# Kernel optimization log

Hardware: AMD Instinct MI355X
Metric: run time of the kernel (lower is better)

## Reference

```python
import jax, jax.numpy as jnp
import numpy as np
import math

B, N, D = 4, 16384, 256
M, H = 64, 8
HD = D // H

def setup_inputs() -> dict:
    key = jax.random.key(0)
    ks = jax.random.split(key, 5)
    s = 1.0 / math.sqrt(D)
    return {
        "x": jax.random.normal(ks[0], (B, N, D), dtype=jnp.float32),
        "Ws": jax.random.normal(ks[1], (M, D), dtype=jnp.float32) * s,
        "bs": jnp.zeros((M,), dtype=jnp.float32),
        "Wqkv": jax.random.normal(ks[2], (3 * D, D), dtype=jnp.float32) * s,
        "Wo": jax.random.normal(ks[3], (D, D), dtype=jnp.float32) * s,
        "bo": jnp.zeros((D,), dtype=jnp.float32),
    }

def reference(x, Ws, bs, Wqkv, Wo, bo):
    # slice weights: softmax over N (dim=1), matching the torch code exactly
    logits = jnp.einsum('bnd,md->bnm', x, Ws) + bs          # [B,N,M]
    weights = jax.nn.softmax(logits, axis=1)                # softmax over N
    # pooling: tokens[b,m,d] = sum_n w[b,n,m] * x[b,n,d]
    tokens = jnp.einsum('bnm,bnd->bmd', weights, x)         # [B,M,D]
    # qkv projection (no bias)
    qkv = jnp.einsum('bmd,ed->bme', tokens, Wqkv)           # [B,M,3D]
    qkv = qkv.reshape(B, M, 3, H, HD)
    q = qkv[:, :, 0].transpose(0, 2, 1, 3)                  # [B,H,M,HD]
    k = qkv[:, :, 1].transpose(0, 2, 1, 3)
    v = qkv[:, :, 2].transpose(0, 2, 1, 3)
    scale = 1.0 / math.sqrt(HD)
    attn = jax.nn.softmax(jnp.einsum('bhmd,bhkd->bhmk', q, k) * scale, axis=-1)
    token_out = jnp.einsum('bhmk,bhkd->bhmd', attn, v)      # [B,H,M,HD]
    token_out = token_out.transpose(0, 2, 1, 3).reshape(B, M, D)
    token_out = jnp.einsum('bmd,ed->bme', token_out, Wo) + bo
    # unpooling: out[b,n,d] = sum_m w[b,n,m] * token_out[b,m,d]
    out = jnp.einsum('bnm,bmd->bnd', weights, token_out)    # [B,N,D]
    return out
```

## Files before the change

### kernel.cpp

```cpp
#include <hip/hip_runtime.h>
#include <math.h>

constexpr int B = 4;
constexpr int N = 16384;
constexpr int D = 256;
constexpr int M = 64;
constexpr int H = 8;

typedef __attribute__((ext_vector_type(8))) short short8;
typedef __attribute__((ext_vector_type(4))) float floatx4;

__device__ __forceinline__ float4 ld4(const float* p) {
  return *reinterpret_cast<const float4*>(p);
}
__device__ __forceinline__ unsigned short f2bf(float f) {
  unsigned u = __float_as_uint(f);
  unsigned r = (u + 0x7fffu + ((u >> 16) & 1u)) >> 16;
  return (unsigned short)r;
}

__global__ __launch_bounds__(256) void k0_prep(
    const float* __restrict__ Ws, const float* __restrict__ Wqkv,
    const float* __restrict__ Wo, unsigned short* __restrict__ WsB,
    unsigned short* __restrict__ WqkvB, unsigned short* __restrict__ WoB) {
  const int g = blockIdx.x * 256 + threadIdx.x;
  const float* src;
  unsigned short* dst;
  int off;
  if (g < 2048) {
    src = Ws; dst = WsB; off = g;
  } else if (g < 26624) {
    src = Wqkv; dst = WqkvB; off = g - 2048;
  } else {
    src = Wo; dst = WoB; off = g - 26624;
  }
  const float4 a = ld4(&src[(size_t)off * 8]);
  const float4 c = ld4(&src[(size_t)off * 8 + 4]);
  unsigned d0 = (unsigned)f2bf(a.x) | ((unsigned)f2bf(a.y) << 16);
  unsigned d1 = (unsigned)f2bf(a.z) | ((unsigned)f2bf(a.w) << 16);
  unsigned d2 = (unsigned)f2bf(c.x) | ((unsigned)f2bf(c.y) << 16);
  unsigned d3 = (unsigned)f2bf(c.z) | ((unsigned)f2bf(c.w) << 16);
  *reinterpret_cast<uint4*>(&dst[(size_t)off * 8]) = make_uint4(d0, d1, d2, d3);
}

__global__ __launch_bounds__(256, 3) void k1_fused(
    const float* __restrict__ x, const unsigned short* __restrict__ WsB,
    const float* __restrict__ bs, unsigned short* __restrict__ En,
    float* __restrict__ denom) {
  __shared__ unsigned short Wt[64][264];
  __shared__ unsigned short Es[64][72];
  __shared__ float red[64];
  const int b = blockIdx.y;
  const int n0 = blockIdx.x * 64;
  const int tid = threadIdx.x;
  const int w = tid >> 6, l = tid & 63;
  const int l15 = l & 15;
  const int q8 = (l >> 4) * 8;
  const int ar = w * 16 + l15;

  float4 fx[16];
  const float* xrow = &x[((size_t)(b * N + n0 + ar)) * D];
#pragma unroll
  for (int ks = 0; ks < 8; ++ks) {
    fx[2 * ks] = ld4(&xrow[ks * 32 + q8]);
    fx[2 * ks + 1] = ld4(&xrow[ks * 32 + q8 + 4]);
  }
#pragma unroll
  for (int p = 0; p < 8; ++p) {
    const int u = p * 256 + tid;
    const int row = u >> 5;
    const int c = (u & 31) * 8;
    *reinterpret_cast<short8*>(&Wt[row][c]) =
        *reinterpret_cast<const short8*>(&WsB[(size_t)row * 256 + c]);
  }
  if (tid < 64) red[tid] = 0.0f;
  __syncthreads();

  short8 afr[8];
#pragma unroll
  for (int ks = 0; ks < 8; ++ks) {
    const float4 a0 = fx[2 * ks], a1 = fx[2 * ks + 1];
    short8 t;
    t[0] = (short)f2bf(a0.x); t[1] = (short)f2bf(a0.y);
    t[2] = (short)f2bf(a0.z); t[3] = (short)f2bf(a0.w);
    t[4] = (short)f2bf(a1.x); t[5] = (short)f2bf(a1.y);
    t[6] = (short)f2bf(a1.z); t[7] = (short)f2bf(a1.w);
    afr[ks] = t;
  }

  floatx4 acc[4] = {{0.f, 0.f, 0.f, 0.f},
                    {0.f, 0.f, 0.f, 0.f},
                    {0.f, 0.f, 0.f, 0.f},
                    {0.f, 0.f, 0.f, 0.f}};
#pragma unroll
  for (int ks = 0; ks < 8; ++ks) {
#pragma unroll
    for (int mt = 0; mt < 4; ++mt) {
      short8 bf = *reinterpret_cast<short8*>(&Wt[mt * 16 + l15][ks * 32 + q8]);
      acc[mt] = __builtin_amdgcn_mfma_f32_16x16x32_bf16(afr[ks], bf, acc[mt], 0, 0, 0);
    }
  }

#pragma unroll
  for (int mt = 0; mt < 4; ++mt) {
    const int m = mt * 16 + l15;
    const float bsm = bs[m];
    float s = 0.0f;
#pragma unroll
    for (int r = 0; r < 4; ++r) {
      const int n = w * 16 + (l >> 4) * 4 + r;
      const float e = expf(acc[mt][r] + bsm);
      s += e;
      Es[n][m] = f2bf(e);
    }
    atomicAdd(&red[m], s);
  }
  __syncthreads();
  if (tid < 64) atomicAdd(&denom[b * M + tid], red[tid]);
#pragma unroll
  for (int p = 0; p < 2; ++p) {
    const int g = p * 256 + tid;
    const int n = g >> 3;
    const int m0 = (g & 7) * 8;
    short8 v = *reinterpret_cast<short8*>(&Es[n][m0]);
    *reinterpret_cast<short8*>(&En[((size_t)(b * N + n0 + n)) * M + m0]) = v;
  }
}

__global__ __launch_bounds__(256) void k2_pool(
    const unsigned short* __restrict__ En, const float* __restrict__ x,
    float* __restrict__ tokens) {
  __shared__ unsigned short Ens[64][66];
  __shared__ unsigned short Xs[64][66];
  const int dt = blockIdx.x, nc = blockIdx.y, b = blockIdx.z;
  const int d0 = dt * 64;
  const int tid = threadIdx.x;
  const int w = tid >> 6, l = tid & 63;
  const int l15 = l & 15;
  const int q8 = (l >> 4) * 8;
  floatx4 acc[4] = {{0.f, 0.f, 0.f, 0.f},
                    {0.f, 0.f, 0.f, 0.f},
                    {0.f, 0.f, 0.f, 0.f},
                    {0.f, 0.f, 0.f, 0.f}};
  for (int kc = 0; kc < 8; ++kc) {
    const int nb = nc * 512 + kc * 64;
    __syncthreads();
#pragma unroll
    for (int p = 0; p < 2; ++p) {
      const int u = p * 256 + tid;
      const int n = u >> 3;
      const int c8 = (u & 7) * 8;
      short8 v = *reinterpret_cast<const short8*>(
          &En[((size_t)(b * N + nb + n)) * M + c8]);
      uint4 uv = *reinterpret_cast<uint4*>(&v);
      unsigned* dp = reinterpret_cast<unsigned*>(&Ens[n][c8]);
      dp[0] = uv.x; dp[1] = uv.y; dp[2] = uv.z; dp[3] = uv.w;
    }
    {
      const int n = tid >> 2;
      const int c16 = (tid & 3) * 16;
      const float* xp = &x[((size_t)(b * N + nb + n)) * D + d0 + c16];
#pragma unroll
      for (int q = 0; q < 4; ++q) {
        float4 v = ld4(xp + q * 4);
        unsigned u0 = (unsigned)f2bf(v.x) | ((unsigned)f2bf(v.y) << 16);
        unsigned u1 = (unsigned)f2bf(v.z) | ((unsigned)f2bf(v.w) << 16);
        unsigned* dp = reinterpret_cast<unsigned*>(&Xs[n][c16 + q * 4]);
        dp[0] = u0; dp[1] = u1;
      }
    }
    __syncthreads();
#pragma unroll
    for (int ks = 0; ks < 2; ++ks) {
      const int nf = ks * 32 + q8;
      short8 a;
#pragma unroll
      for (int j = 0; j < 8; ++j) a[j] = (short)Ens[nf + j][w * 16 + l15];
#pragma unroll
      for (int dtile = 0; dtile < 4; ++dtile) {
        short8 bf;
#pragma unroll
        for (int j = 0; j < 8; ++j) bf[j] = (short)Xs[nf + j][dtile * 16 + l15];
        acc[dtile] =
            __builtin_amdgcn_mfma_f32_16x16x32_bf16(a, bf, acc[dtile], 0, 0, 0);
      }
    }
  }
#pragma unroll
  for (int dtile = 0; dtile < 4; ++dtile)
#pragma unroll
    for (int r = 0; r < 4; ++r) {
      const int m = w * 16 + (l >> 4) * 4 + r;
      const int d = d0 + dtile * 16 + (l & 15);
      atomicAdd(&tokens[((size_t)(b * M + m)) * D + d], acc[dtile][r]);
    }
}

__global__ __launch_bounds__(256) void k_proj(
    const float* __restrict__ A, const unsigned short* __restrict__ WB,
    const float* __restrict__ bias, const float* __restrict__ denom,
    float* __restrict__ OutF, unsigned short* __restrict__ OutT, const int EC,
    const int mode) {
  __shared__ unsigned short At[64][264];
  __shared__ unsigned short Wt[64][264];
  __shared__ float Cs[64][68];
  const int et = blockIdx.x;
  const int b = blockIdx.y;
  const int tid = threadIdx.x;
  const int w = tid >> 6, l = tid & 63;
#pragma unroll
  for (int p = 0; p < 16; ++p) {
    const int i = p * 256 + tid;
    const int row = i >> 6;
    const int c4 = (i & 63) * 4;
    float4 av = ld4(&A[((size_t)(b * M + row)) * D + c4]);
    unsigned a0 = (unsigned)f2bf(av.x) | ((unsigned)f2bf(av.y) << 16);
    unsigned a1 = (unsigned)f2bf(av.z) | ((unsigned)f2bf(av.w) << 16);
    *reinterpret_cast<uint2*>(&At[row][c4]) = make_uint2(a0, a1);
  }
#pragma unroll
  for (int p = 0; p < 8; ++p) {
    const int u = p * 256 + tid;
    const int row = u >> 5;
    const int c = (u & 31) * 8;
    *reinterpret_cast<short8*>(&Wt[row][c]) =
        *reinterpret_cast<const short8*>(&WB[((size_t)(et * 64 + row)) * 256 + c]);
  }
  __syncthreads();
  floatx4 acc[4] = {{0.f, 0.f, 0.f, 0.f},
                    {0.f, 0.f, 0.f, 0.f},
                    {0.f, 0.f, 0.f, 0.f},
                    {0.f, 0.f, 0.f, 0.f}};
  const int ar = w * 16 + (l & 15);
  const int q8 = (l >> 4) * 8;
#pragma unroll
  for (int ks = 0; ks < 8; ++ks) {
    short8 a = *reinterpret_cast<short8*>(&At[ar][ks * 32 + q8]);
#pragma unroll
    for (int mt = 0; mt < 4; ++mt) {
      short8 bf = *reinterpret_cast<short8*>(&Wt[mt * 16 + (l & 15)][ks * 32 + q8]);
      acc[mt] = __builtin_amdgcn_mfma_f32_16x16x32_bf16(a, bf, acc[mt], 0, 0, 0);
    }
  }
  if (mode == 0) {
#pragma unroll
    for (int mt = 0; mt < 4; ++mt) {
#pragma unroll
      for (int r = 0; r < 4; ++r) {
        const int row = w * 16 + (l >> 4) * 4 + r;
        const float rcp = 1.0f / denom[b * M + row];
        const int e = et * 64 + mt * 16 + (l & 15);
        OutF[((size_t)(b * M + row)) * EC + e] = acc[mt][r] * rcp;
      }
    }
  } else {
#pragma unroll
    for (int mt = 0; mt < 4; ++mt) {
#pragma unroll
      for (int r = 0; r < 4; ++r) {
        const int row = w * 16 + (l >> 4) * 4 + r;
        const float rcp = 1.0f / denom[b * M + row];
        const int el = mt * 16 + (l & 15);
        const float bv = bias[et * 64 + el];
        Cs[row][el] = (acc[mt][r] + bv) * rcp;
      }
    }
    __syncthreads();
#pragma unroll
    for (int p = 0; p < 2; ++p) {
      const int g = p * 256 + tid;
      const int e = g >> 3;
      const int m0 = (g & 7) * 8;
      unsigned short bu[8];
#pragma unroll
      for (int k = 0; k < 8; ++k) bu[k] = f2bf(Cs[m0 + k][e]);
      uint4 pk;
      pk.x = (unsigned)bu[0] | ((unsigned)bu[1] << 16);
      pk.y = (unsigned)bu[2] | ((unsigned)bu[3] << 16);
      pk.z = (unsigned)bu[4] | ((unsigned)bu[5] << 16);
      pk.w = (unsigned)bu[6] | ((unsigned)bu[7] << 16);
      *reinterpret_cast<uint4*>(
          &OutT[((size_t)(b * D + et * 64 + e)) * M + m0]) = pk;
    }
  }
}

__global__ __launch_bounds__(256) void k4_attn(
    const float* __restrict__ qkv, float* __restrict__ attn_o) {
  __shared__ float qt[32][68];
  __shared__ float kt[32][68];
  __shared__ float vv[64][36];
  __shared__ float P[64][68];
  const int b = blockIdx.x >> 3;
  const int h = blockIdx.x & 7;
  const int tid = threadIdx.x;
  for (int i = tid; i < 512; i += 256) {
    const int m = i >> 3;
    const int c4 = (i & 7) * 4;
    const float* base = &qkv[((size_t)(b * M + m)) * 768 + h * 32 + c4];
    float4 q4 = ld4(base);
    float4 k4 = ld4(base + 256);
    float4 v4 = ld4(base + 512);
    qt[c4 + 0][m] = q4.x; qt[c4 + 1][m] = q4.y; qt[c4 + 2][m] = q4.z; qt[c4 + 3][m] = q4.w;
    kt[c4 + 0][m] = k4.x; kt[c4 + 1][m] = k4.y; kt[c4 + 2][m] = k4.z; kt[c4 + 3][m] = k4.w;
    *reinterpret_cast<float4*>(&vv[m][c4]) = v4;
  }
  __syncthreads();
  {
    const int tm4 = (tid & 15) * 4;
    const int tn4 = (tid >> 4) * 4;
    float acc[4][4] = {};
    for (int k = 0; k < 32; ++k) {
      float4 a4 = ld4(&qt[k][tn4]);
      float4 b4 = ld4(&kt[k][tm4]);
#pragma unroll
      for (int i = 0; i < 4; ++i) {
        const float av = (i == 0) ? a4.x : (i == 1) ? a4.y : (i == 2) ? a4.z : a4.w;
        acc[i][0] = fmaf(av, b4.x, acc[i][0]);
        acc[i][1] = fmaf(av, b4.y, acc[i][1]);
        acc[i][2] = fmaf(av, b4.z, acc[i][2]);
        acc[i][3] = fmaf(av, b4.w, acc[i][3]);
      }
    }
    const float scale = 0.17677669529663687f;
#pragma unroll
    for (int i = 0; i < 4; ++i)
      *reinterpret_cast<float4*>(&P[tn4 + i][tm4]) =
          make_float4(acc[i][0] * scale, acc[i][1] * scale, acc[i][2] * scale,
                      acc[i][3] * scale);
  }
  __syncthreads();
  if (tid < 64) {
    float mx = -1e30f;
    for (int j = 0; j < 64; ++j) mx = fmaxf(mx, P[tid][j]);
    float s = 0.0f;
    for (int j = 0; j < 64; ++j) {
      const float e = expf(P[tid][j] - mx);
      P[tid][j] = e;
      s += e;
    }
    const float r = 1.0f / s;
    for (int j = 0; j < 64; ++j) P[tid][j] *= r;
  }
  __syncthreads();
  if (tid < 128) {
    const int i0 = (tid >> 3) * 4;
    const int c0 = (tid & 7) * 4;
    float o[4][4] = {};
    for (int j = 0; j < 64; ++j) {
      float4 v4 = ld4(&vv[j][c0]);
#pragma unroll
      for (int ii = 0; ii < 4; ++ii) {
        const float p = P[i0 + ii][j];
        o[ii][0] = fmaf(p, v4.x, o[ii][0]);
        o[ii][1] = fmaf(p, v4.y, o[ii][1]);
        o[ii][2] = fmaf(p, v4.z, o[ii][2]);
        o[ii][3] = fmaf(p, v4.w, o[ii][3]);
      }
    }
#pragma unroll
    for (int ii = 0; ii < 4; ++ii)
      *reinterpret_cast<float4*>(
          &attn_o[((size_t)(b * M + i0 + ii)) * D + h * 32 + c0]) =
          make_float4(o[ii][0], o[ii][1], o[ii][2], o[ii][3]);
  }
}

__global__ __launch_bounds__(256) void k6_unpool(
    const unsigned short* __restrict__ En, const unsigned short* __restrict__ TpT,
    float* __restrict__ out) {
  __shared__ unsigned short EnS[64][72];
  __shared__ unsigned short TpS[64][72];
  const int dt = blockIdx.x, nt = blockIdx.y, b = blockIdx.z;
  const int n0 = nt * 64, d0 = dt * 64;
  const int tid = threadIdx.x;
  const int w = tid >> 6, l = tid & 63;
#pragma unroll
  for (int p = 0; p < 2; ++p) {
    const int g = p * 256 + tid;
    const int row = g >> 3;
    const int c8 = (g & 7) * 8;
    *reinterpret_cast<short8*>(&EnS[row][c8]) =
        *reinterpret_cast<const short8*>(
            &En[((size_t)(b * N + n0 + row)) * M + c8]);
    *reinterpret_cast<short8*>(&TpS[row][c8]) =
        *reinterpret_cast<const short8*>(
            &TpT[((size_t)(b * D + d0 + row)) * M + c8]);
  }
  __syncthreads();
  floatx4 acc[4] = {{0.f, 0.f, 0.f, 0.f},
                    {0.f, 0.f, 0.f, 0.f},
                    {0.f, 0.f, 0.f, 0.f},
                    {0.f, 0.f, 0.f, 0.f}};
  const int q8 = (l >> 4) * 8;
#pragma unroll
  for (int ks = 0; ks < 2; ++ks) {
    short8 a = *reinterpret_cast<short8*>(&EnS[w * 16 + (l & 15)][ks * 32 + q8]);
#pragma unroll
    for (int dtile = 0; dtile < 4; ++dtile) {
      short8 bf = *reinterpret_cast<short8*>(
          &TpS[dtile * 16 + (l & 15)][ks * 32 + q8]);
      acc[dtile] =
          __builtin_amdgcn_mfma_f32_16x16x32_bf16(a, bf, acc[dtile], 0, 0, 0);
    }
  }
#pragma unroll
  for (int dtile = 0; dtile < 4; ++dtile)
#pragma unroll
    for (int r = 0; r < 4; ++r) {
      const int n = n0 + w * 16 + (l >> 4) * 4 + r;
      const int d = d0 + dtile * 16 + (l & 15);
      out[((size_t)(b * N + n)) * D + d] = acc[dtile][r];
    }
}

extern "C" void kernel_launch(void* const* d_in, const int* in_sizes, int n_in,
                              void* d_out, int out_size, void* d_ws,
                              size_t ws_size, hipStream_t stream) {
  const float* x = (const float*)d_in[0];
  const float* Ws = (const float*)d_in[1];
  const float* bs = (const float*)d_in[2];
  const float* Wqkv = (const float*)d_in[3];
  const float* Wo = (const float*)d_in[4];
  const float* bo = (const float*)d_in[5];
  float* out = (float*)d_out;

  char* p = (char*)d_ws;
  unsigned short* En = (unsigned short*)p;    p += (size_t)B * N * M * 2;
  unsigned short* TpT = (unsigned short*)p;   p += (size_t)B * D * M * 2;
  float* denom = (float*)p;                   p += (size_t)B * M * 4;
  float* tokens = (float*)p;                  p += (size_t)B * M * D * 4;
  float* qkv = (float*)p;                     p += (size_t)B * M * 3 * D * 4;
  float* attn_o = (float*)p;                  p += (size_t)B * M * D * 4;
  unsigned short* WsB = (unsigned short*)p;   p += (size_t)M * D * 2;
  unsigned short* WqkvB = (unsigned short*)p; p += (size_t)3 * D * D * 2;
  unsigned short* WoB = (unsigned short*)p;   p += (size_t)D * D * 2;

  hipMemsetAsync(denom, 0, (size_t)B * M * sizeof(float), stream);
  hipMemsetAsync(tokens, 0, (size_t)B * M * D * sizeof(float), stream);

  k0_prep<<<dim3(136), 256, 0, stream>>>(Ws, Wqkv, Wo, WsB, WqkvB, WoB);
  k1_fused<<<dim3(N / 64, B), 256, 0, stream>>>(x, WsB, bs, En, denom);
  k2_pool<<<dim3(D / 64, N / 512, B), 256, 0, stream>>>(En, x, tokens);
  k_proj<<<dim3(12, B), 256, 0, stream>>>(tokens, WqkvB, nullptr, denom, qkv,
                                          nullptr, 768, 0);
  k4_attn<<<dim3(B * H), 256, 0, stream>>>(qkv, attn_o);
  k_proj<<<dim3(4, B), 256, 0, stream>>>(attn_o, WoB, bo, denom, nullptr, TpT,
                                         256, 1);
  k6_unpool<<<dim3(D / 64, N / 64, B), 256, 0, stream>>>(En, TpT, out);
}
```

Before: 185.8 us.

## Fold memsets into prep kernel, enlarge k1 blocks, transpose x tile in pool

```diff
diff --git a/kernel.cpp b/kernel.cpp
--- a/kernel.cpp
+++ b/kernel.cpp
@@ -22,8 +22,13 @@
 __global__ __launch_bounds__(256) void k0_prep(
     const float* __restrict__ Ws, const float* __restrict__ Wqkv,
     const float* __restrict__ Wo, unsigned short* __restrict__ WsB,
-    unsigned short* __restrict__ WqkvB, unsigned short* __restrict__ WoB) {
+    unsigned short* __restrict__ WqkvB, unsigned short* __restrict__ WoB,
+    float* __restrict__ denom, float* __restrict__ tokens) {
   const int g = blockIdx.x * 256 + threadIdx.x;
+  if (g < 32768)
+    *reinterpret_cast<float2*>(&tokens[g * 2]) = make_float2(0.f, 0.f);
+  if (g < 128)
+    *reinterpret_cast<float2*>(&denom[g * 2]) = make_float2(0.f, 0.f);
   const float* src;
   unsigned short* dst;
   int off;
@@ -43,15 +48,14 @@
   *reinterpret_cast<uint4*>(&dst[(size_t)off * 8]) = make_uint4(d0, d1, d2, d3);
 }
 
-__global__ __launch_bounds__(256, 3) void k1_fused(
+__global__ __launch_bounds__(512, 4) void k1_fused(
     const float* __restrict__ x, const unsigned short* __restrict__ WsB,
     const float* __restrict__ bs, unsigned short* __restrict__ En,
     float* __restrict__ denom) {
   __shared__ unsigned short Wt[64][264];
-  __shared__ unsigned short Es[64][72];
   __shared__ float red[64];
   const int b = blockIdx.y;
-  const int n0 = blockIdx.x * 64;
+  const int n0 = blockIdx.x * 128;
   const int tid = threadIdx.x;
   const int w = tid >> 6, l = tid & 63;
   const int l15 = l & 15;
@@ -66,15 +70,14 @@
     fx[2 * ks + 1] = ld4(&xrow[ks * 32 + q8 + 4]);
   }
 #pragma unroll
-  for (int p = 0; p < 8; ++p) {
-    const int u = p * 256 + tid;
+  for (int p = 0; p < 4; ++p) {
+    const int u = p * 512 + tid;
     const int row = u >> 5;
     const int c = (u & 31) * 8;
     *reinterpret_cast<short8*>(&Wt[row][c]) =
         *reinterpret_cast<const short8*>(&WsB[(size_t)row * 256 + c]);
   }
   if (tid < 64) red[tid] = 0.0f;
-  __syncthreads();
 
   short8 afr[8];
 #pragma unroll
@@ -87,6 +90,7 @@
     t[6] = (short)f2bf(a1.z); t[7] = (short)f2bf(a1.w);
     afr[ks] = t;
   }
+  __syncthreads();
 
   floatx4 acc[4] = {{0.f, 0.f, 0.f, 0.f},
                     {0.f, 0.f, 0.f, 0.f},
@@ -111,27 +115,19 @@
       const int n = w * 16 + (l >> 4) * 4 + r;
       const float e = expf(acc[mt][r] + bsm);
       s += e;
-      Es[n][m] = f2bf(e);
+      En[((size_t)(b * N + n0 + n)) * M + m] = f2bf(e);
     }
     atomicAdd(&red[m], s);
   }
   __syncthreads();
   if (tid < 64) atomicAdd(&denom[b * M + tid], red[tid]);
-#pragma unroll
-  for (int p = 0; p < 2; ++p) {
-    const int g = p * 256 + tid;
-    const int n = g >> 3;
-    const int m0 = (g & 7) * 8;
-    short8 v = *reinterpret_cast<short8*>(&Es[n][m0]);
-    *reinterpret_cast<short8*>(&En[((size_t)(b * N + n0 + n)) * M + m0]) = v;
-  }
 }
 
 __global__ __launch_bounds__(256) void k2_pool(
     const unsigned short* __restrict__ En, const float* __restrict__ x,
     float* __restrict__ tokens) {
-  __shared__ unsigned short Ens[64][66];
-  __shared__ unsigned short Xs[64][66];
+  __shared__ unsigned short Ens[64][70];
+  __shared__ unsigned short XsT[64][72];
   const int dt = blockIdx.x, nc = blockIdx.y, b = blockIdx.z;
   const int d0 = dt * 64;
   const int tid = threadIdx.x;
@@ -142,8 +138,8 @@
                     {0.f, 0.f, 0.f, 0.f},
                     {0.f, 0.f, 0.f, 0.f},
                     {0.f, 0.f, 0.f, 0.f}};
-  for (int kc = 0; kc < 8; ++kc) {
-    const int nb = nc * 512 + kc * 64;
+  for (int kc = 0; kc < 4; ++kc) {
+    const int nb = nc * 256 + kc * 64;
     __syncthreads();
 #pragma unroll
     for (int p = 0; p < 2; ++p) {
@@ -163,10 +159,10 @@
 #pragma unroll
       for (int q = 0; q < 4; ++q) {
         float4 v = ld4(xp + q * 4);
-        unsigned u0 = (unsigned)f2bf(v.x) | ((unsigned)f2bf(v.y) << 16);
-        unsigned u1 = (unsigned)f2bf(v.z) | ((unsigned)f2bf(v.w) << 16);
-        unsigned* dp = reinterpret_cast<unsigned*>(&Xs[n][c16 + q * 4]);
-        dp[0] = u0; dp[1] = u1;
+        XsT[c16 + q * 4 + 0][n] = f2bf(v.x);
+        XsT[c16 + q * 4 + 1][n] = f2bf(v.y);
+        XsT[c16 + q * 4 + 2][n] = f2bf(v.z);
+        XsT[c16 + q * 4 + 3][n] = f2bf(v.w);
       }
     }
     __syncthreads();
@@ -178,9 +174,7 @@
       for (int j = 0; j < 8; ++j) a[j] = (short)Ens[nf + j][w * 16 + l15];
 #pragma unroll
       for (int dtile = 0; dtile < 4; ++dtile) {
-        short8 bf;
-#pragma unroll
-        for (int j = 0; j < 8; ++j) bf[j] = (short)Xs[nf + j][dtile * 16 + l15];
+        short8 bf = *reinterpret_cast<short8*>(&XsT[dtile * 16 + l15][nf]);
         acc[dtile] =
             __builtin_amdgcn_mfma_f32_16x16x32_bf16(a, bf, acc[dtile], 0, 0, 0);
       }
@@ -436,12 +430,10 @@
   unsigned short* WqkvB = (unsigned short*)p; p += (size_t)3 * D * D * 2;
   unsigned short* WoB = (unsigned short*)p;   p += (size_t)D * D * 2;
 
-  hipMemsetAsync(denom, 0, (size_t)B * M * sizeof(float), stream);
-  hipMemsetAsync(tokens, 0, (size_t)B * M * D * sizeof(float), stream);
-
-  k0_prep<<<dim3(136), 256, 0, stream>>>(Ws, Wqkv, Wo, WsB, WqkvB, WoB);
-  k1_fused<<<dim3(N / 64, B), 256, 0, stream>>>(x, WsB, bs, En, denom);
-  k2_pool<<<dim3(D / 64, N / 512, B), 256, 0, stream>>>(En, x, tokens);
+  k0_prep<<<dim3(136), 256, 0, stream>>>(Ws, Wqkv, Wo, WsB, WqkvB, WoB,
+                                         denom, tokens);
+  k1_fused<<<dim3(N / 128, B), 512, 0, stream>>>(x, WsB, bs, En, denom);
+  k2_pool<<<dim3(D / 64, N / 256, B), 256, 0, stream>>>(En, x, tokens);
   k_proj<<<dim3(12, B), 256, 0, stream>>>(tokens, WqkvB, nullptr, denom, qkv,
                                           nullptr, 768, 0);
   k4_attn<<<dim3(B * H), 256, 0, stream>>>(qkv, attn_o);
```

Result: faster. 180.1 us (-3.1%).
